# Kernel tuning notes

Measured on AMD Instinct MI355X. Metric: run time of the kernel, lower is better.

The kernel has to match this reference:

```python
import jax, jax.numpy as jnp
import numpy as np

N, E, IN_FEATS, H = 20000, 320000, 512, 64
EPS = 1e-5  # BatchNorm eps


def setup_inputs() -> dict:
    key = jax.random.key(0)
    ks = iter(jax.random.split(key, 64))
    rn = lambda *s: jax.random.normal(next(ks), s, dtype=jnp.float32)
    d = {}
    d["x"] = rn(N, IN_FEATS)
    d["edge_index"] = jax.random.randint(next(ks), (2, E), 0, N)
    d["Wm"] = rn(IN_FEATS, H) * 0.05; d["bm"] = rn(H) * 0.05
    d["Wc"] = rn(IN_FEATS, H) * 0.05; d["bc"] = rn(H) * 0.05
    d["Wg1"] = rn(H, 2 * H) * 0.05;     d["bg1"] = rn(2 * H) * 0.05
    d["Wg2"] = rn(2 * H, 2 * H) * 0.05; d["bg2"] = rn(2 * H) * 0.05
    d["Wg3"] = rn(2 * H, 4 * H) * 0.05; d["bg3"] = rn(4 * H) * 0.05
    for name, cin in (("e1", 8 * H), ("e2", 4 * H), ("e3", 4 * H)):
        d[name + "_gamma"] = 1.0 + rn(cin) * 0.1
        d[name + "_beta"] = rn(cin) * 0.1
        d[name + "_mean"] = rn(cin) * 0.1
        d[name + "_var"] = jax.random.uniform(next(ks), (cin,), dtype=jnp.float32) + 0.5
        d[name + "_W"] = rn(cin, 2 * H) * 0.05
    d["Wfc"] = rn(2 * H, 1) * 0.05; d["bfc"] = rn(1) * 0.05
    return d


def _gcn(x, W, b, src, dst, n):
    """PyG GCNConv: self-loops + symmetric normalization + sum aggregation."""
    h = x @ W  # [N, out]
    loop = jnp.arange(n)
    s = jnp.concatenate([src, loop])
    d = jnp.concatenate([dst, loop])
    deg = jax.ops.segment_sum(jnp.ones(s.shape[0], h.dtype), d, num_segments=n)
    dinv = jnp.where(deg > 0, jax.lax.rsqrt(deg), 0.0)
    msg = h[s] * (dinv[s] * dinv[d])[:, None]  # gather + normalize
    return jax.ops.segment_sum(msg, d, num_segments=n) + b


def _edge_conv(x, gamma, beta, mean, var, W, src, dst, n):
    """PyG EdgeConv with LinearPathPreact nn (BN->ReLU->Linear), max aggregation."""
    xi = x[dst]
    xj = x[src]
    feat = jnp.concatenate([xi, xj - xi], axis=-1)  # [E, 2*C]
    h = (feat - mean) * jax.lax.rsqrt(var + EPS) * gamma + beta  # BN (eval stats)
    h = jnp.maximum(h, 0.0) @ W  # ReLU -> Linear(bias=False)
    out = jax.ops.segment_max(h, dst, num_segments=n)
    return jnp.where(jnp.isfinite(out), out, 0.0)  # empty segments -> 0


def reference(x, edge_index, Wm, bm, Wc, bc, Wg1, bg1, Wg2, bg2, Wg3, bg3,
              e1_gamma, e1_beta, e1_mean, e1_var, e1_W,
              e2_gamma, e2_beta, e2_mean, e2_var, e2_W,
              e3_gamma, e3_beta, e3_mean, e3_var, e3_W,
              Wfc, bfc):
    n = x.shape[0]
    src, dst = edge_index[0], edge_index[1]
    x0_main = x @ Wm + bm
    x0 = x @ Wc + bc
    x0 = x0.at[0::4].set(x0_main[0::4])  # main-person rows use the main projection
    g = _gcn(x0, Wg1, bg1, src, dst, n)
    g = _gcn(g, Wg2, bg2, src, dst, n)
    g = _gcn(g, Wg3, bg3, src, dst, n)
    h = _edge_conv(g, e1_gamma, e1_beta, e1_mean, e1_var, e1_W, src, dst, n)
    h = _edge_conv(h, e2_gamma, e2_beta, e2_mean, e2_var, e2_W, src, dst, n)
    h = _edge_conv(h, e3_gamma, e3_beta, e3_mean, e3_var, e3_W, src, dst, n)
    return h @ Wfc + bfc  # [N, 1]
```

## Files before the change

### kernel.cpp

```cpp
#include <hip/hip_runtime.h>

#define DEVINL __device__ __forceinline__

constexpr int N_NODES  = 20000;
constexpr int N_EDGES  = 320000;
constexpr int IN_FEATS = 512;

static_assert(N_EDGES % 128 == 0, "edge tiling assumes E % 128 == 0");
static_assert(N_NODES % 16 == 0, "proj assumes N % 16 == 0");

typedef __attribute__((ext_vector_type(8))) short short8;
typedef __attribute__((ext_vector_type(4))) float f32x4;

DEVINL unsigned enc_f32(float v) {
  unsigned b = __float_as_uint(v);
  return (b & 0x80000000u) ? ~b : (b | 0x80000000u);
}
DEVINL float dec_f32(unsigned e) {
  unsigned b = (e & 0x80000000u) ? (e & 0x7FFFFFFFu) : ~e;
  return __uint_as_float(b);
}

DEVINL unsigned short bf16_rne(float f) {
  unsigned u = __float_as_uint(f);
  u += 0x7FFFu + ((u >> 16) & 1u);
  return (unsigned short)(u >> 16);
}
DEVINL void split_bf16(float v, unsigned short& h, unsigned short& l) {
  h = bf16_rne(v);
  float hf = __uint_as_float((unsigned)h << 16);
  l = bf16_rne(v - hf);
}

DEVINL void glds16(const unsigned short* g, unsigned short* l) {
  __builtin_amdgcn_global_load_lds(
      (const __attribute__((address_space(1))) unsigned int*)g,
      (__attribute__((address_space(3))) unsigned int*)l, 16, 0, 0);
}

__global__ void hist_kernel(const int* __restrict__ dst, int* __restrict__ cnt, int e) {
  int i = blockIdx.x * 256 + threadIdx.x;
  if (i < e) atomicAdd(&cnt[dst[i]], 1);
}
__global__ void dinv_kernel(const int* __restrict__ cnt, float* __restrict__ dinv, int n) {
  int i = blockIdx.x * 256 + threadIdx.x;
  if (i < n) dinv[i] = rsqrtf((float)cnt[i] + 1.0f);
}
__global__ void __launch_bounds__(256)
scan_p1(const int* __restrict__ cnt, int* __restrict__ rp, int* __restrict__ bsum, int n) {
  __shared__ int buf[256];
  int i = blockIdx.x * 256 + threadIdx.x;
  int v = (i < n) ? cnt[i] : 0;
  buf[threadIdx.x] = v;
  __syncthreads();
  for (int off = 1; off < 256; off <<= 1) {
    int t = (threadIdx.x >= off) ? buf[threadIdx.x - off] : 0;
    __syncthreads();
    buf[threadIdx.x] += t;
    __syncthreads();
  }
  if (i < n) rp[i] = buf[threadIdx.x] - v;
  if (threadIdx.x == 255) bsum[blockIdx.x] = buf[255];
}
__global__ void __launch_bounds__(256)
scan_p2(int* __restrict__ bsum, int nb) {
  __shared__ int buf[256];
  int v = (threadIdx.x < nb) ? bsum[threadIdx.x] : 0;
  buf[threadIdx.x] = v;
  __syncthreads();
  for (int off = 1; off < 256; off <<= 1) {
    int t = (threadIdx.x >= off) ? buf[threadIdx.x - off] : 0;
    __syncthreads();
    buf[threadIdx.x] += t;
    __syncthreads();
  }
  if (threadIdx.x < nb) bsum[threadIdx.x] = buf[threadIdx.x] - v;
}
__global__ void __launch_bounds__(256)
scan_p3(int* __restrict__ rp, const int* __restrict__ bsum, int* __restrict__ cursor,
        int n, int e) {
  int i = blockIdx.x * 256 + threadIdx.x;
  if (i < n) {
    int v = rp[i] + bsum[blockIdx.x];
    rp[i] = v;
    cursor[i] = v;
  }
  if (i == 0) rp[n] = e;
}
__global__ void scatter_edges_kernel(const int* __restrict__ src, const int* __restrict__ dst,
                                     int* __restrict__ cursor, int* __restrict__ ssrc,
                                     int* __restrict__ sdst, int e) {
  int i = blockIdx.x * 256 + threadIdx.x;
  if (i < e) {
    int d = dst[i];
    int pos = atomicAdd(&cursor[d], 1);
    ssrc[pos] = src[i];
    sdst[pos] = d;
  }
}

DEVINL void bn1(const float* g, const float* b, const float* m, const float* v,
                float* sc, float* sh, int i) {
  float s = g[i] * rsqrtf(v[i] + 1e-5f);
  sc[i] = s;
  sh[i] = b[i] - m[i] * s;
}
__global__ void bn_prep_all(const float* g1, const float* b1, const float* m1, const float* v1,
                            float* sc1, float* sh1, const float* g2, const float* b2,
                            const float* m2, const float* v2, float* sc2, float* sh2,
                            const float* g3, const float* b3, const float* m3, const float* v3,
                            float* sc3, float* sh3) {
  int i = blockIdx.x * 256 + threadIdx.x;
  if (i < 512) bn1(g1, b1, m1, v1, sc1, sh1, i);
  else if (i < 768) bn1(g2, b2, m2, v2, sc2, sh2, i - 512);
  else if (i < 1024) bn1(g3, b3, m3, v3, sc3, sh3, i - 768);
}

DEVINL void wfrag1(const float* W, unsigned short* out, int e) {
  int k = e >> 7, c = e & 127;
  unsigned short h, l;
  split_bf16(W[e], h, l);
  int chunk = k >> 5, kq = (k >> 3) & 3, j = k & 7, ct = c >> 4, n = c & 15;
  int frag = (ct * 4 + kq) * 16 + n;
  size_t o = (size_t)chunk * 8192 + frag * 8 + j;
  out[o] = h;
  out[o + 4096] = l;
}
__global__ void wfrag_all(const float* __restrict__ e1W, const float* __restrict__ e2W,
                          const float* __restrict__ e3W, unsigned short* b1p,
                          unsigned short* b1q, unsigned short* b2p, unsigned short* b2q,
                          unsigned short* b3p, unsigned short* b3q) {
  int g = blockIdx.x * 256 + threadIdx.x;
  if (g < 32768) wfrag1(e1W, b1p, g);
  else if (g < 65536) wfrag1(e1W + 32768, b1q, g - 32768);
  else if (g < 81920) wfrag1(e2W, b2p, g - 65536);
  else if (g < 98304) wfrag1(e2W + 16384, b2q, g - 81920);
  else if (g < 114688) wfrag1(e3W, b3p, g - 98304);
  else wfrag1(e3W + 16384, b3q, g - 114688);
}

__global__ void combine_kernel(unsigned* __restrict__ Q, const float* __restrict__ P,
                               float* __restrict__ H, int n, int zq) {
  int i = blockIdx.x * 256 + threadIdx.x;
  if (i < n) {
    unsigned e = Q[i];
    H[i] = e ? (P[i] + dec_f32(e)) : 0.f;
    if (zq) Q[i] = 0u;
  }
}

__global__ void __launch_bounds__(256)
proj_kernel(const float* __restrict__ X, const float* __restrict__ Wm,
            const float* __restrict__ bm, const float* __restrict__ Wc,
            const float* __restrict__ bc, const float* __restrict__ dinv,
            float* __restrict__ Y0) {
  __shared__ float xs[16][IN_FEATS];
  int tid = threadIdx.x;
  int rowBase = blockIdx.x * 16;
  for (int i = 0; i < 8; ++i) {
    int idx = i * 256 + tid;
    int r = idx >> 7, kq = idx & 127;
    *reinterpret_cast<float4*>(&xs[r][kq * 4]) =
        *reinterpret_cast<const float4*>(X + (size_t)(rowBase + r) * IN_FEATS + kq * 4);
  }
  __syncthreads();
  int r4 = tid >> 6;
  int j = tid & 63;
  const float* W = (r4 == 0) ? Wm : Wc;
  float a0 = 0.f, a1 = 0.f, a2 = 0.f, a3 = 0.f;
#pragma unroll 4
  for (int k = 0; k < IN_FEATS; ++k) {
    float w = W[k * 64 + j];
    a0 = fmaf(xs[r4][k], w, a0);
    a1 = fmaf(xs[r4 + 4][k], w, a1);
    a2 = fmaf(xs[r4 + 8][k], w, a2);
    a3 = fmaf(xs[r4 + 12][k], w, a3);
  }
  float b = (r4 == 0) ? bm[j] : bc[j];
  int r0 = rowBase + r4;
  Y0[(size_t)r0 * 64 + j] = (a0 + b) * dinv[r0];
  Y0[(size_t)(r0 + 4) * 64 + j] = (a1 + b) * dinv[r0 + 4];
  Y0[(size_t)(r0 + 8) * 64 + j] = (a2 + b) * dinv[r0 + 8];
  Y0[(size_t)(r0 + 12) * 64 + j] = (a3 + b) * dinv[r0 + 12];
}

template <int LOGF4>
__global__ void __launch_bounds__(256)
agg_kernel(const float* __restrict__ Y, const int* __restrict__ row_ptr,
           const int* __restrict__ ssrc, const float* __restrict__ dinv,
           float* __restrict__ Z, int n) {
  constexpr int F4 = 1 << LOGF4;
  int g = blockIdx.x * 256 + threadIdx.x;
  int d = g >> LOGF4, c4 = g & (F4 - 1);
  if (d >= n) return;
  const float4* Yp = (const float4*)Y;
  float4 a = Yp[(size_t)d * F4 + c4];
  float ax = a.x, ay = a.y, az = a.z, aw = a.w;
  int e = row_ptr[d], end = row_ptr[d + 1];
  for (; e + 7 < end; e += 8) {
    int s[8];
#pragma unroll
    for (int i = 0; i < 8; ++i) s[i] = ssrc[e + i];
    float4 v[8];
#pragma unroll
    for (int i = 0; i < 8; ++i) v[i] = Yp[(size_t)s[i] * F4 + c4];
#pragma unroll
    for (int i = 0; i < 8; ++i) {
      ax += v[i].x; ay += v[i].y; az += v[i].z; aw += v[i].w;
    }
  }
  for (; e < end; ++e) {
    float4 v = Yp[(size_t)ssrc[e] * F4 + c4];
    ax += v.x; ay += v.y; az += v.z; aw += v.w;
  }
  float s = dinv[d];
  ((float4*)Z)[(size_t)d * F4 + c4] = make_float4(ax * s, ay * s, az * s, aw * s);
}

template <int K, int F, bool SCALE>
__global__ void __launch_bounds__(256)
gemm_kernel(const float* __restrict__ X, const float* __restrict__ W,
            const float* __restrict__ bias, const float* __restrict__ dinv,
            float* __restrict__ H, int n) {
  __shared__ float Xs[64][K + 1];
  __shared__ float Ws[K][65];
  int tid = threadIdx.x;
  int rowBase = blockIdx.x * 64;
  int colBase = blockIdx.y * 64;
  for (int idx = tid; idx < 64 * K; idx += 256) {
    int r = idx / K, k = idx % K;
    int row = rowBase + r;
    Xs[r][k] = (row < n) ? X[(size_t)row * K + k] : 0.f;
  }
  for (int idx = tid; idx < K * 64; idx += 256) {
    int k = idx >> 6, c = idx & 63;
    Ws[k][c] = W[(size_t)k * F + colBase + c];
  }
  __syncthreads();
  int tx = tid & 15, ty = tid >> 4;
  float acc[4][4] = {};
  for (int k = 0; k < K; ++k) {
    float a[4], b[4];
#pragma unroll
    for (int r = 0; r < 4; ++r) a[r] = Xs[ty * 4 + r][k];
#pragma unroll
    for (int c = 0; c < 4; ++c) b[c] = Ws[k][tx * 4 + c];
#pragma unroll
    for (int r = 0; r < 4; ++r)
#pragma unroll
      for (int c = 0; c < 4; ++c) acc[r][c] = fmaf(a[r], b[c], acc[r][c]);
  }
#pragma unroll
  for (int r = 0; r < 4; ++r) {
    int row = rowBase + ty * 4 + r;
    if (row < n) {
      float di = SCALE ? dinv[row] : 1.0f;
#pragma unroll
      for (int c = 0; c < 4; ++c) {
        int col = colBase + tx * 4 + c;
        float v = acc[r][c] + bias[col];
        H[(size_t)row * F + col] = SCALE ? v * di : v;
      }
    }
  }
}

DEVINL void proc8(const float4& va, const float4& vb, const float4& sa, const float4& sb,
                  const float4& ha, const float4& hb, short8& hi, short8& lo) {
  float f[8] = {va.x, va.y, va.z, va.w, vb.x, vb.y, vb.z, vb.w};
  float s[8] = {sa.x, sa.y, sa.z, sa.w, sb.x, sb.y, sb.z, sb.w};
  float t[8] = {ha.x, ha.y, ha.z, ha.w, hb.x, hb.y, hb.z, hb.w};
#pragma unroll
  for (int j = 0; j < 8; ++j) {
    float v = fmaxf(fmaf(f[j], s[j], t[j]), 0.f);
    unsigned short hh, ll;
    split_bf16(v, hh, ll);
    hi[j] = (short)hh;
    lo[j] = (short)ll;
  }
}

template <int C, bool EDGE>
__global__ void __launch_bounds__(256, 2)
ec_mfma_kernel(const float* __restrict__ X, const int* __restrict__ ssrc,
               const int* __restrict__ sdst, const float* __restrict__ scale,
               const float* __restrict__ shift, const unsigned short* __restrict__ Bfrag,
               unsigned* __restrict__ outU, float* __restrict__ outP, int nrows) {
  constexpr int NCH = C / 32;
  constexpr int HALVES = C / 128;
  __shared__ unsigned short Bmat[32768];
  __shared__ float ss[2 * C];
  __shared__ int de_s[128];
  const int tid = threadIdx.x, lane = tid & 63, wv = tid >> 6;
  const int q = lane >> 4, mn = lane & 15;
  const int base = blockIdx.x * 128;
  const int koff = q * 8;
  const int lr0 = wv * 32 + mn, lr1 = lr0 + 16;

  int id0, id1, is0 = 0, is1 = 0;
  if (EDGE) {
    if (tid < 128) de_s[tid] = sdst[base + tid];
    is0 = ssrc[base + lr0];
    id0 = sdst[base + lr0];
    is1 = ssrc[base + lr1];
    id1 = sdst[base + lr1];
  } else {
    id0 = min(base + lr0, nrows - 1);
    id1 = min(base + lr1, nrows - 1);
  }
  const float* pd0 = X + (size_t)id0 * C + koff;
  const float* pd1 = X + (size_t)id1 * C + koff;
  const float* ps0 = EDGE ? X + (size_t)is0 * C + koff : nullptr;
  const float* ps1 = EDGE ? X + (size_t)is1 * C + koff : nullptr;

  f32x4 acc[8][2];
#pragma unroll
  for (int i = 0; i < 8; ++i) {
    acc[i][0] = (f32x4)0.f;
    acc[i][1] = (f32x4)0.f;
  }

  float4 A[3][8];
#define LOAD_A(cc, slot)                                   \
  {                                                        \
    const int kk_ = (cc) * 32;                             \
    A[slot][0] = *(const float4*)(pd0 + kk_);              \
    A[slot][1] = *(const float4*)(pd0 + kk_ + 4);          \
    A[slot][2] = *(const float4*)(pd1 + kk_);              \
    A[slot][3] = *(const float4*)(pd1 + kk_ + 4);          \
    if (EDGE) {                                            \
      A[slot][4] = *(const float4*)(ps0 + kk_);            \
      A[slot][5] = *(const float4*)(ps0 + kk_ + 4);        \
      A[slot][6] = *(const float4*)(ps1 + kk_);            \
      A[slot][7] = *(const float4*)(ps1 + kk_ + 4);        \
    }                                                      \
  }

  LOAD_A(0, 0);
  if (NCH > 1) LOAD_A(1, 1);
  {
    constexpr int NF4 = C / 4;
    if (tid < NF4)
      ((float4*)ss)[tid] = ((const float4*)scale)[tid];
    else if (tid < 2 * NF4)
      ((float4*)(ss + C))[tid - NF4] = ((const float4*)shift)[tid - NF4];
  }
  {
    const unsigned short* bs = Bfrag + lane * 8;
#pragma unroll
    for (int i = 0; i < 16; ++i) {
      int seg = wv * 16 + i;
      glds16(bs + seg * 512, Bmat + seg * 512);
    }
  }
  __syncthreads();

#pragma unroll
  for (int h = 0; h < HALVES; ++h) {
    if (h > 0) {
      __syncthreads();
      const unsigned short* bs = Bfrag + 32768 + lane * 8;
#pragma unroll
      for (int i = 0; i < 16; ++i) {
        int seg = wv * 16 + i;
        glds16(bs + seg * 512, Bmat + seg * 512);
      }
      __syncthreads();
    }
#pragma unroll
    for (int cc = 0; cc < 4; ++cc) {
      const int c = h * 4 + cc;
      const int kc = c * 32;
      if (c + 2 < NCH) LOAD_A(c + 2, (c + 2) % 3);
      float4 sca = *(const float4*)&ss[kc + koff];
      float4 scb = *(const float4*)&ss[kc + koff + 4];
      float4 sha = *(const float4*)&ss[C + kc + koff];
      float4 shb = *(const float4*)&ss[C + kc + koff + 4];
      const int sl = c % 3;
      float4 u0, u1, u2, u3;
      if (EDGE) {
        u0 = make_float4(A[sl][4].x - A[sl][0].x, A[sl][4].y - A[sl][0].y,
                         A[sl][4].z - A[sl][0].z, A[sl][4].w - A[sl][0].w);
        u1 = make_float4(A[sl][5].x - A[sl][1].x, A[sl][5].y - A[sl][1].y,
                         A[sl][5].z - A[sl][1].z, A[sl][5].w - A[sl][1].w);
        u2 = make_float4(A[sl][6].x - A[sl][2].x, A[sl][6].y - A[sl][2].y,
                         A[sl][6].z - A[sl][2].z, A[sl][6].w - A[sl][2].w);
        u3 = make_float4(A[sl][7].x - A[sl][3].x, A[sl][7].y - A[sl][3].y,
                         A[sl][7].z - A[sl][3].z, A[sl][7].w - A[sl][3].w);
      } else {
        u0 = A[sl][0]; u1 = A[sl][1]; u2 = A[sl][2]; u3 = A[sl][3];
      }
      short8 ah0, al0, ah1, al1;
      proc8(u0, u1, sca, scb, sha, shb, ah0, al0);
      proc8(u2, u3, sca, scb, sha, shb, ah1, al1);
      const unsigned short* Bc = Bmat + cc * 8192;
#pragma unroll
      for (int ct = 0; ct < 8; ++ct) {
        int fi = ct * 64 + lane;
        short8 bh = *(const short8*)(Bc + fi * 8);
        short8 bl = *(const short8*)(Bc + 4096 + fi * 8);
        acc[ct][0] = __builtin_amdgcn_mfma_f32_16x16x32_bf16(ah0, bh, acc[ct][0], 0, 0, 0);
        acc[ct][1] = __builtin_amdgcn_mfma_f32_16x16x32_bf16(ah1, bh, acc[ct][1], 0, 0, 0);
        acc[ct][0] = __builtin_amdgcn_mfma_f32_16x16x32_bf16(ah0, bl, acc[ct][0], 0, 0, 0);
        acc[ct][1] = __builtin_amdgcn_mfma_f32_16x16x32_bf16(ah1, bl, acc[ct][1], 0, 0, 0);
        acc[ct][0] = __builtin_amdgcn_mfma_f32_16x16x32_bf16(al0, bh, acc[ct][0], 0, 0, 0);
        acc[ct][1] = __builtin_amdgcn_mfma_f32_16x16x32_bf16(al1, bh, acc[ct][1], 0, 0, 0);
      }
    }
  }
#undef LOAD_A

  if (EDGE) {
#pragma unroll
    for (int ct = 0; ct < 8; ++ct) {
      int f = ct * 16 + mn;
      float mv = 0.f;
      int prev = -1;
#pragma unroll
      for (int g = 0; g < 2; ++g) {
        int e0 = wv * 32 + g * 16 + q * 4;
#pragma unroll
        for (int r = 0; r < 4; ++r) {
          int d = de_s[e0 + r];
          float v = acc[ct][g][r];
          if (prev < 0) {
            prev = d; mv = v;
          } else if (d == prev) {
            mv = fmaxf(mv, v);
          } else {
            atomicMax(&outU[(size_t)prev * 128 + f], enc_f32(mv));
            prev = d; mv = v;
          }
        }
      }
      atomicMax(&outU[(size_t)prev * 128 + f], enc_f32(mv));
    }
  } else {
#pragma unroll
    for (int ct = 0; ct < 8; ++ct) {
      int f = ct * 16 + mn;
#pragma unroll
      for (int g = 0; g < 2; ++g) {
        int r0 = base + wv * 32 + g * 16 + q * 4;
#pragma unroll
        for (int r = 0; r < 4; ++r) {
          int row = r0 + r;
          if (row < nrows) outP[(size_t)row * 128 + f] = acc[ct][g][r];
        }
      }
    }
  }
}

__global__ void __launch_bounds__(256)
fc_kernel(const float* __restrict__ Hf, const float* __restrict__ Wfc,
          const float* __restrict__ bfc, float* __restrict__ out, int n) {
  int g = blockIdx.x * 256 + threadIdx.x;
  int node = g >> 6, lane = g & 63;
  if (node >= n) return;
  float v = fmaf(Hf[(size_t)node * 128 + lane], Wfc[lane],
                 Hf[(size_t)node * 128 + 64 + lane] * Wfc[64 + lane]);
#pragma unroll
  for (int off = 32; off > 0; off >>= 1) v += __shfl_down(v, off);
  if (lane == 0) out[node] = v + bfc[0];
}

extern "C" void kernel_launch(void* const* d_in, const int* in_sizes, int n_in,
                              void* d_out, int out_size, void* d_ws, size_t ws_size,
                              hipStream_t stream) {
  const float* x   = (const float*)d_in[0];
  const int*   ei  = (const int*)d_in[1];
  const float* Wm  = (const float*)d_in[2];
  const float* bm  = (const float*)d_in[3];
  const float* Wc  = (const float*)d_in[4];
  const float* bc  = (const float*)d_in[5];
  const float* Wg1 = (const float*)d_in[6];
  const float* bg1 = (const float*)d_in[7];
  const float* Wg2 = (const float*)d_in[8];
  const float* bg2 = (const float*)d_in[9];
  const float* Wg3 = (const float*)d_in[10];
  const float* bg3 = (const float*)d_in[11];
  const float* e1g = (const float*)d_in[12];
  const float* e1b = (const float*)d_in[13];
  const float* e1m = (const float*)d_in[14];
  const float* e1v = (const float*)d_in[15];
  const float* e1W = (const float*)d_in[16];
  const float* e2g = (const float*)d_in[17];
  const float* e2b = (const float*)d_in[18];
  const float* e2m = (const float*)d_in[19];
  const float* e2v = (const float*)d_in[20];
  const float* e2W = (const float*)d_in[21];
  const float* e3g = (const float*)d_in[22];
  const float* e3b = (const float*)d_in[23];
  const float* e3m = (const float*)d_in[24];
  const float* e3v = (const float*)d_in[25];
  const float* e3W = (const float*)d_in[26];
  const float* Wfc = (const float*)d_in[27];
  const float* bfc = (const float*)d_in[28];

  const int* src = ei;
  const int* dst = ei + N_EDGES;

  float* ws   = (float*)d_ws;
  float* dinv = ws;
  float* y0   = dinv + N_NODES;
  float* zb   = y0 + (size_t)N_NODES * 64;
  float* yb   = zb + (size_t)N_NODES * 128;
  float* G    = yb + (size_t)N_NODES * 128;
  float* sc1  = G + (size_t)N_NODES * 256;
  float* sh1  = sc1 + 512;
  float* sc2  = sh1 + 512;
  float* sh2  = sc2 + 256;
  float* sc3  = sh2 + 256;
  float* sh3  = sc3 + 256;
  unsigned short* bf1p = (unsigned short*)(sh3 + 256);
  unsigned short* bf1q = bf1p + 65536;
  unsigned short* bf2p = bf1q + 65536;
  unsigned short* bf2q = bf2p + 32768;
  unsigned short* bf3p = bf2q + 32768;
  unsigned short* bf3q = bf3p + 32768;
  int* cnt     = (int*)(bf3q + 32768);
  int* row_ptr = cnt + N_NODES;
  int* cursor  = row_ptr + N_NODES + 1;
  int* bsum    = cursor + N_NODES;
  int* ssrc    = bsum + 256;
  int* sdst    = ssrc + N_EDGES;

  float*    Pbuf = zb;
  unsigned* Qbuf = (unsigned*)yb;

  hipMemsetAsync(cnt, 0, N_NODES * sizeof(int), stream);
  hist_kernel<<<N_EDGES / 256, 256, 0, stream>>>(dst, cnt, N_EDGES);
  dinv_kernel<<<79, 256, 0, stream>>>(cnt, dinv, N_NODES);
  scan_p1<<<79, 256, 0, stream>>>(cnt, row_ptr, bsum, N_NODES);
  scan_p2<<<1, 256, 0, stream>>>(bsum, 79);
  scan_p3<<<79, 256, 0, stream>>>(row_ptr, bsum, cursor, N_NODES, N_EDGES);
  scatter_edges_kernel<<<N_EDGES / 256, 256, 0, stream>>>(src, dst, cursor, ssrc, sdst,
                                                          N_EDGES);

  bn_prep_all<<<4, 256, 0, stream>>>(e1g, e1b, e1m, e1v, sc1, sh1, e2g, e2b, e2m, e2v, sc2,
                                     sh2, e3g, e3b, e3m, e3v, sc3, sh3);
  wfrag_all<<<512, 256, 0, stream>>>(e1W, e2W, e3W, bf1p, bf1q, bf2p, bf2q, bf3p, bf3q);

  proj_kernel<<<N_NODES / 16, 256, 0, stream>>>(x, Wm, bm, Wc, bc, dinv, y0);
  dim3 grid2(313, 2), grid4(313, 4);
  agg_kernel<4><<<N_NODES * 16 / 256, 256, 0, stream>>>(y0, row_ptr, ssrc, dinv, zb, N_NODES);
  gemm_kernel<64, 128, true><<<grid2, 256, 0, stream>>>(zb, Wg1, bg1, dinv, yb, N_NODES);
  agg_kernel<5><<<N_NODES * 32 / 256, 256, 0, stream>>>(yb, row_ptr, ssrc, dinv, zb, N_NODES);
  gemm_kernel<128, 128, true><<<grid2, 256, 0, stream>>>(zb, Wg2, bg2, dinv, yb, N_NODES);
  agg_kernel<5><<<N_NODES * 32 / 256, 256, 0, stream>>>(yb, row_ptr, ssrc, dinv, zb, N_NODES);
  gemm_kernel<128, 256, false><<<grid4, 256, 0, stream>>>(zb, Wg3, bg3, dinv, G, N_NODES);

  const int NODE_BLOCKS = (N_NODES + 127) / 128;
  const int EDGE_BLOCKS = N_EDGES / 128;
  const int NB_ELEM     = N_NODES * 128 / 256;

  float* H1 = G;
  float* H2 = G + (size_t)N_NODES * 128;
  float* H3 = G;

  hipMemsetAsync(Qbuf, 0, (size_t)N_NODES * 128 * 4, stream);
  ec_mfma_kernel<256, false><<<NODE_BLOCKS, 256, 0, stream>>>(
      G, nullptr, nullptr, sc1, sh1, bf1p, nullptr, Pbuf, N_NODES);
  ec_mfma_kernel<256, true><<<EDGE_BLOCKS, 256, 0, stream>>>(
      G, ssrc, sdst, sc1 + 256, sh1 + 256, bf1q, Qbuf, nullptr, N_NODES);
  combine_kernel<<<NB_ELEM, 256, 0, stream>>>(Qbuf, Pbuf, H1, N_NODES * 128, 1);

  ec_mfma_kernel<128, false><<<NODE_BLOCKS, 256, 0, stream>>>(
      H1, nullptr, nullptr, sc2, sh2, bf2p, nullptr, Pbuf, N_NODES);
  ec_mfma_kernel<128, true><<<EDGE_BLOCKS, 256, 0, stream>>>(
      H1, ssrc, sdst, sc2 + 128, sh2 + 128, bf2q, Qbuf, nullptr, N_NODES);
  combine_kernel<<<NB_ELEM, 256, 0, stream>>>(Qbuf, Pbuf, H2, N_NODES * 128, 1);

  ec_mfma_kernel<128, false><<<NODE_BLOCKS, 256, 0, stream>>>(
      H2, nullptr, nullptr, sc3, sh3, bf3p, nullptr, Pbuf, N_NODES);
  ec_mfma_kernel<128, true><<<EDGE_BLOCKS, 256, 0, stream>>>(
      H2, ssrc, sdst, sc3 + 128, sh3 + 128, bf3q, Qbuf, nullptr, N_NODES);
  combine_kernel<<<NB_ELEM, 256, 0, stream>>>(Qbuf, Pbuf, H3, N_NODES * 128, 0);

  fc_kernel<<<N_NODES * 64 / 256, 256, 0, stream>>>(H3, Wfc, bfc, (float*)d_out, N_NODES);
}
```

Before: 796.3 us.

## Collapse linear GCN stack into 64-wide propagations plus rank-one bias terms

The three GCN layers have no nonlinearity between them, so the weight matrices are multiplied together once (W1·W2·W3) and the normalized propagation is applied three times on the 64-wide projected features. The biases are carried through as rank-one corrections built from per-node vectors u1 and u2, which are computed with scalar aggregation kernels. This replaces two 128-wide aggregations and three GEMMs with 64-wide aggregations and a single GEMM, at the cost of a few small setup kernels and a different floating-point summation order.

```diff
diff --git a/kernel.cpp b/kernel.cpp
--- a/kernel.cpp
+++ b/kernel.cpp
@@ -42,9 +42,14 @@
   int i = blockIdx.x * 256 + threadIdx.x;
   if (i < e) atomicAdd(&cnt[dst[i]], 1);
 }
-__global__ void dinv_kernel(const int* __restrict__ cnt, float* __restrict__ dinv, int n) {
-  int i = blockIdx.x * 256 + threadIdx.x;
-  if (i < n) dinv[i] = rsqrtf((float)cnt[i] + 1.0f);
+__global__ void dinv_kernel(const int* __restrict__ cnt, float* __restrict__ dinv,
+                            float* __restrict__ dinv2, int n) {
+  int i = blockIdx.x * 256 + threadIdx.x;
+  if (i < n) {
+    float s = rsqrtf((float)cnt[i] + 1.0f);
+    dinv[i] = s;
+    dinv2[i] = s * s;
+  }
 }
 __global__ void __launch_bounds__(256)
 scan_p1(const int* __restrict__ cnt, int* __restrict__ rp, int* __restrict__ bsum, int n) {
@@ -97,6 +102,40 @@
     ssrc[pos] = src[i];
     sdst[pos] = d;
   }
+}
+
+__global__ void uvec1_kernel(const int* __restrict__ row_ptr, const int* __restrict__ ssrc,
+                             const float* __restrict__ dinv, float* __restrict__ u1,
+                             float* __restrict__ w1, int n) {
+  int d = blockIdx.x * 256 + threadIdx.x;
+  if (d >= n) return;
+  float s = dinv[d];
+  float acc = s;
+  int e = row_ptr[d], end = row_ptr[d + 1];
+  for (; e < end; ++e) acc += dinv[ssrc[e]];
+  float u = s * acc;
+  u1[d] = u;
+  w1[d] = s * u;
+}
+__global__ void uvec2_kernel(const int* __restrict__ row_ptr, const int* __restrict__ ssrc,
+                             const float* __restrict__ dinv, const float* __restrict__ w1,
+                             float* __restrict__ u2, int n) {
+  int d = blockIdx.x * 256 + threadIdx.x;
+  if (d >= n) return;
+  float acc = w1[d];
+  int e = row_ptr[d], end = row_ptr[d + 1];
+  for (; e < end; ++e) acc += w1[ssrc[e]];
+  u2[d] = dinv[d] * acc;
+}
+
+__global__ void smallmm(const float* __restrict__ A, const float* __restrict__ B,
+                        float* __restrict__ Cc, int m, int k, int n) {
+  int i = blockIdx.x * 256 + threadIdx.x;
+  if (i >= m * n) return;
+  int r = i / n, c = i % n;
+  float acc = 0.f;
+  for (int kk = 0; kk < k; ++kk) acc = fmaf(A[r * k + kk], B[kk * n + c], acc);
+  Cc[i] = acc;
 }
 
 DEVINL void bn1(const float* g, const float* b, const float* m, const float* v,
@@ -187,7 +226,7 @@
 template <int LOGF4>
 __global__ void __launch_bounds__(256)
 agg_kernel(const float* __restrict__ Y, const int* __restrict__ row_ptr,
-           const int* __restrict__ ssrc, const float* __restrict__ dinv,
+           const int* __restrict__ ssrc, const float* __restrict__ mfac,
            float* __restrict__ Z, int n) {
   constexpr int F4 = 1 << LOGF4;
   int g = blockIdx.x * 256 + threadIdx.x;
@@ -213,15 +252,16 @@
     float4 v = Yp[(size_t)ssrc[e] * F4 + c4];
     ax += v.x; ay += v.y; az += v.z; aw += v.w;
   }
-  float s = dinv[d];
+  float s = mfac[d];
   ((float4*)Z)[(size_t)d * F4 + c4] = make_float4(ax * s, ay * s, az * s, aw * s);
 }
 
-template <int K, int F, bool SCALE>
 __global__ void __launch_bounds__(256)
-gemm_kernel(const float* __restrict__ X, const float* __restrict__ W,
-            const float* __restrict__ bias, const float* __restrict__ dinv,
-            float* __restrict__ H, int n) {
+gemm_rank1_kernel(const float* __restrict__ X, const float* __restrict__ W,
+                  const float* __restrict__ b3, const float* __restrict__ u1,
+                  const float* __restrict__ u2, const float* __restrict__ c1,
+                  const float* __restrict__ c2, float* __restrict__ H, int n) {
+  constexpr int K = 64, F = 256;
   __shared__ float Xs[64][K + 1];
   __shared__ float Ws[K][65];
   int tid = threadIdx.x;
@@ -254,12 +294,12 @@
   for (int r = 0; r < 4; ++r) {
     int row = rowBase + ty * 4 + r;
     if (row < n) {
-      float di = SCALE ? dinv[row] : 1.0f;
+      float du2 = u2[row], du1 = u1[row];
 #pragma unroll
       for (int c = 0; c < 4; ++c) {
         int col = colBase + tx * 4 + c;
-        float v = acc[r][c] + bias[col];
-        H[(size_t)row * F + col] = SCALE ? v * di : v;
+        float v = acc[r][c] + du2 * c1[col] + du1 * c2[col] + b3[col];
+        H[(size_t)row * F + col] = v;
       }
     }
   }
@@ -501,55 +541,69 @@
   const int* src = ei;
   const int* dst = ei + N_EDGES;
 
-  float* ws   = (float*)d_ws;
-  float* dinv = ws;
-  float* y0   = dinv + N_NODES;
-  float* zb   = y0 + (size_t)N_NODES * 64;
-  float* yb   = zb + (size_t)N_NODES * 128;
-  float* G    = yb + (size_t)N_NODES * 128;
-  float* sc1  = G + (size_t)N_NODES * 256;
-  float* sh1  = sc1 + 512;
-  float* sc2  = sh1 + 512;
-  float* sh2  = sc2 + 256;
-  float* sc3  = sh2 + 256;
-  float* sh3  = sc3 + 256;
+  float* ws    = (float*)d_ws;
+  float* dinv  = ws;
+  float* dinv2 = dinv + N_NODES;
+  float* u1    = dinv2 + N_NODES;
+  float* w1    = u1 + N_NODES;
+  float* u2    = w1 + N_NODES;
+  float* y0    = u2 + N_NODES;
+  float* za    = y0 + (size_t)N_NODES * 64;
+  float* zb    = za + (size_t)N_NODES * 64;
+  float* PQ    = zb + (size_t)N_NODES * 64;
+  float* G     = PQ + (size_t)N_NODES * 256;
+  float* sc1   = G + (size_t)N_NODES * 256;
+  float* sh1   = sc1 + 512;
+  float* sc2   = sh1 + 512;
+  float* sh2   = sc2 + 256;
+  float* sc3   = sh2 + 256;
+  float* sh3   = sc3 + 256;
   unsigned short* bf1p = (unsigned short*)(sh3 + 256);
   unsigned short* bf1q = bf1p + 65536;
   unsigned short* bf2p = bf1q + 65536;
   unsigned short* bf2q = bf2p + 32768;
   unsigned short* bf3p = bf2q + 32768;
   unsigned short* bf3q = bf3p + 32768;
-  int* cnt     = (int*)(bf3q + 32768);
+  float* W23   = (float*)(bf3q + 32768);
+  float* W123  = W23 + 32768;
+  float* c1    = W123 + 16384;
+  float* c2    = c1 + 256;
+  int* cnt     = (int*)(c2 + 256);
   int* row_ptr = cnt + N_NODES;
   int* cursor  = row_ptr + N_NODES + 1;
   int* bsum    = cursor + N_NODES;
   int* ssrc    = bsum + 256;
   int* sdst    = ssrc + N_EDGES;
 
-  float*    Pbuf = zb;
-  unsigned* Qbuf = (unsigned*)yb;
+  float*    Pbuf = PQ;
+  unsigned* Qbuf = (unsigned*)(PQ + (size_t)N_NODES * 128);
 
   hipMemsetAsync(cnt, 0, N_NODES * sizeof(int), stream);
   hist_kernel<<<N_EDGES / 256, 256, 0, stream>>>(dst, cnt, N_EDGES);
-  dinv_kernel<<<79, 256, 0, stream>>>(cnt, dinv, N_NODES);
+  dinv_kernel<<<79, 256, 0, stream>>>(cnt, dinv, dinv2, N_NODES);
   scan_p1<<<79, 256, 0, stream>>>(cnt, row_ptr, bsum, N_NODES);
   scan_p2<<<1, 256, 0, stream>>>(bsum, 79);
   scan_p3<<<79, 256, 0, stream>>>(row_ptr, bsum, cursor, N_NODES, N_EDGES);
   scatter_edges_kernel<<<N_EDGES / 256, 256, 0, stream>>>(src, dst, cursor, ssrc, sdst,
                                                           N_EDGES);
 
+  smallmm<<<128, 256, 0, stream>>>(Wg2, Wg3, W23, 128, 128, 256);
+  smallmm<<<64, 256, 0, stream>>>(Wg1, W23, W123, 64, 128, 256);
+  smallmm<<<1, 256, 0, stream>>>(bg1, W23, c1, 1, 128, 256);
+  smallmm<<<1, 256, 0, stream>>>(bg2, Wg3, c2, 1, 128, 256);
+  uvec1_kernel<<<79, 256, 0, stream>>>(row_ptr, ssrc, dinv, u1, w1, N_NODES);
+  uvec2_kernel<<<79, 256, 0, stream>>>(row_ptr, ssrc, dinv, w1, u2, N_NODES);
+
   bn_prep_all<<<4, 256, 0, stream>>>(e1g, e1b, e1m, e1v, sc1, sh1, e2g, e2b, e2m, e2v, sc2,
                                      sh2, e3g, e3b, e3m, e3v, sc3, sh3);
   wfrag_all<<<512, 256, 0, stream>>>(e1W, e2W, e3W, bf1p, bf1q, bf2p, bf2q, bf3p, bf3q);
 
   proj_kernel<<<N_NODES / 16, 256, 0, stream>>>(x, Wm, bm, Wc, bc, dinv, y0);
-  dim3 grid2(313, 2), grid4(313, 4);
-  agg_kernel<4><<<N_NODES * 16 / 256, 256, 0, stream>>>(y0, row_ptr, ssrc, dinv, zb, N_NODES);
-  gemm_kernel<64, 128, true><<<grid2, 256, 0, stream>>>(zb, Wg1, bg1, dinv, yb, N_NODES);
-  agg_kernel<5><<<N_NODES * 32 / 256, 256, 0, stream>>>(yb, row_ptr, ssrc, dinv, zb, N_NODES);
-  gemm_kernel<128, 128, true><<<grid2, 256, 0, stream>>>(zb, Wg2, bg2, dinv, yb, N_NODES);
-  agg_kernel<5><<<N_NODES * 32 / 256, 256, 0, stream>>>(yb, row_ptr, ssrc, dinv, zb, N_NODES);
-  gemm_kernel<128, 256, false><<<grid4, 256, 0, stream>>>(zb, Wg3, bg3, dinv, G, N_NODES);
+  agg_kernel<4><<<N_NODES * 16 / 256, 256, 0, stream>>>(y0, row_ptr, ssrc, dinv2, za, N_NODES);
+  agg_kernel<4><<<N_NODES * 16 / 256, 256, 0, stream>>>(za, row_ptr, ssrc, dinv2, zb, N_NODES);
+  agg_kernel<4><<<N_NODES * 16 / 256, 256, 0, stream>>>(zb, row_ptr, ssrc, dinv, za, N_NODES);
+  dim3 grid4(313, 4);
+  gemm_rank1_kernel<<<grid4, 256, 0, stream>>>(za, W123, bg3, u1, u2, c1, c2, G, N_NODES);
 
   const int NODE_BLOCKS = (N_NODES + 127) / 128;
   const int EDGE_BLOCKS = N_EDGES / 128;
```

After: 802.4 us. No clear change (+0.8%).
